# Optimization experiments

Hardware: AMD Instinct MI355X
Metric: run time of the kernel (lower is better)

Reference implementation:

```python
import jax, jax.numpy as jnp
import numpy as np
from jax import lax

B, S, C, H, T = 64, 256, 64, 512, 128  # batch, enc seq, coord_dims, hidden, target_len

def _lstm_step(Wih, Whh, b, h, c, xt):
    # PyTorch gate order: i, f, g, o
    g = xt @ Wih.T + h @ Whh.T + b
    i, f, gg, o = jnp.split(g, 4, axis=-1)
    i = jax.nn.sigmoid(i); f = jax.nn.sigmoid(f)
    gg = jnp.tanh(gg); o = jax.nn.sigmoid(o)
    c = f * c + i * gg
    h = o * jnp.tanh(c)
    return h, c

def _lstm_layer(x_seq, Wih, Whh, b):
    # x_seq: [B, S, D] -> outputs [B, S, H], final (h, c)
    Bsz = x_seq.shape[0]
    h0 = jnp.zeros((Bsz, Whh.shape[1]), x_seq.dtype)
    c0 = jnp.zeros_like(h0)
    def step(carry, xt):
        h, c = carry
        h, c = _lstm_step(Wih, Whh, b, h, c, xt)
        return (h, c), h
    (hT, cT), ys = lax.scan(step, (h0, c0), x_seq.swapaxes(0, 1))
    return ys.swapaxes(0, 1), hT, cT

def setup_inputs() -> dict:
    key = jax.random.key(0)
    ks = jax.random.split(key, 16)
    s = 1.0 / np.sqrt(H)
    def u(k, shape):
        return jax.random.uniform(k, shape, jnp.float32, -s, s)
    inp = {"x": jax.random.normal(ks[0], (B, S, C), jnp.float32), "target_len": T}
    inp["enc_Wih0"] = u(ks[1], (4 * H, C)); inp["enc_Whh0"] = u(ks[2], (4 * H, H)); inp["enc_b0"] = u(ks[3], (4 * H,))
    inp["enc_Wih1"] = u(ks[4], (4 * H, H)); inp["enc_Whh1"] = u(ks[5], (4 * H, H)); inp["enc_b1"] = u(ks[6], (4 * H,))
    inp["dec_Wih0"] = u(ks[7], (4 * H, C)); inp["dec_Whh0"] = u(ks[8], (4 * H, H)); inp["dec_b0"] = u(ks[9], (4 * H,))
    inp["dec_Wih1"] = u(ks[10], (4 * H, H)); inp["dec_Whh1"] = u(ks[11], (4 * H, H)); inp["dec_b1"] = u(ks[12], (4 * H,))
    inp["lin_W"] = u(ks[13], (C, H)); inp["lin_b"] = u(ks[14], (C,))
    return inp

def reference(x, enc_Wih0, enc_Whh0, enc_b0, enc_Wih1, enc_Whh1, enc_b1,
              dec_Wih0, dec_Whh0, dec_b0, dec_Wih1, dec_Whh1, dec_b1,
              lin_W, lin_b, target_len):
    # ---- encoder: 2-layer LSTM over full sequence ----
    y0, h0, c0 = _lstm_layer(x, enc_Wih0, enc_Whh0, enc_b0)
    _, h1, c1 = _lstm_layer(y0, enc_Wih1, enc_Whh1, enc_b1)
    dec_in0 = x[:, -1, :]  # [B, C]
    def step(carry, _):
        xin, h0_, c0_, h1_, c1_ = carry
        h0n, c0n = _lstm_step(dec_Wih0, dec_Whh0, dec_b0, h0_, c0_, xin)
        h1n, c1n = _lstm_step(dec_Wih1, dec_Whh1, dec_b1, h1_, c1_, h0n)
        out = h1n @ lin_W.T + lin_b  # [B, C]
        return (out, h0n, c0n, h1n, c1n), out
    _, outs = lax.scan(step, (dec_in0, h0, c0, h1, c1), None, length=target_len)
    return outs.swapaxes(0, 1)  # [B, target_len, C]
```

## Files before the change

### kernel.cpp

```cpp
#include <hip/hip_runtime.h>

typedef _Float16 f16;
typedef _Float16 f16x4 __attribute__((ext_vector_type(4)));
typedef _Float16 f16x8 __attribute__((ext_vector_type(8)));
typedef float    f32x4 __attribute__((ext_vector_type(4)));

#define MFMA16(a,b,c) __builtin_amdgcn_mfma_f32_16x16x32_f16((a),(b),(c),0,0,0)

constexpr unsigned NB = 64, NS = 256, NC = 64, NH = 512, NT = 128;
constexpr unsigned HSLOT = NB * NH;

constexpr unsigned OFF_WX   = 0;
constexpr unsigned OFF_WLIN = OFF_WX   + NB*NS*NC*2;
constexpr unsigned OFF_EH0  = OFF_WLIN + NC*NH*2;
constexpr unsigned OFF_EH1  = OFF_EH0  + 2*HSLOT*2;
constexpr unsigned OFF_DH0  = OFF_EH1  + 2*HSLOT*2;
constexpr unsigned OFF_DH1  = OFF_DH0  + 2*HSLOT*2;
constexpr unsigned OFF_BAR  = OFF_DH1  + 2*HSLOT*2;


__global__ void prep_convert(const float* __restrict__ x,
                             const float* __restrict__ linw,
                             char* __restrict__ ws)
{
    unsigned rel = blockIdx.x * 256u + threadIdx.x;
    if (rel < 65536u) {
        unsigned t = rel >> 8, c4 = (rel >> 4) & 15u, b0 = (rel & 15u) << 2;
        #pragma unroll
        for (unsigned j = 0; j < 4; ++j) {
            float4 v = ((const float4*)x)[(b0 + j) * 4096u + t * 16u + c4];
            f16x4 o; o[0]=(f16)v.x; o[1]=(f16)v.y; o[2]=(f16)v.z; o[3]=(f16)v.w;
            ((f16x4*)(ws + OFF_WX))[t * 1024u + c4 * 64u + b0 + j] = o;
        }
    } else if ((rel -= 65536u) < 8192u) {
        float4 v = ((const float4*)linw)[rel];
        f16x4 o; o[0]=(f16)v.x; o[1]=(f16)v.y; o[2]=(f16)v.z; o[3]=(f16)v.w;
        ((f16x4*)(ws + OFF_WLIN))[rel] = o;
    } else if ((rel -= 8192u) < 32768u) {
        f16x8 z = {};
        ((f16x8*)(ws + OFF_EH0))[rel] = z;
    } else if ((rel -= 32768u) < 512u) {
        int4 z; z.x = z.y = z.z = z.w = 0;
        ((int4*)(ws + OFF_BAR))[rel] = z;
    }
}


__device__ __forceinline__ float sigm(float v)   { return 1.f / (1.f + __expf(-v)); }
__device__ __forceinline__ float tanh_f(float v) { return 2.f / (1.f + __expf(-2.f * v)) - 1.f; }

__device__ __forceinline__ void h_store8(f16* p, f16x4 v)
{
    union { unsigned long long u; f16x4 h; } c; c.h = v;
    __hip_atomic_store((unsigned long long*)p, c.u, __ATOMIC_RELAXED, __HIP_MEMORY_SCOPE_AGENT);
}
__device__ __forceinline__ f16x4 h_load8(const f16* p)
{
    unsigned long long v = __hip_atomic_load((const unsigned long long*)p,
                                             __ATOMIC_RELAXED, __HIP_MEMORY_SCOPE_AGENT);
    union { unsigned long long u; f16x4 h; } c; c.u = v;
    return c.h;
}
__device__ __forceinline__ f16x8 h_load_blk(const f16* slot, int kr, int m)
{
    const f16* p = slot + ((kr >> 2) << 8) + (m << 2);
    f16x4 a = h_load8(p);
    f16x4 b = h_load8(p + 256);
    f16x8 r;
    r[0]=a[0]; r[1]=a[1]; r[2]=a[2]; r[3]=a[3];
    r[4]=b[0]; r[5]=b[1]; r[6]=b[2]; r[7]=b[3];
    return r;
}

__device__ __forceinline__ void grid_barrier(int* bar, int wg, int tid, int& bgen)
{
    __syncthreads();
    if (tid == 0) {
        const int g = wg >> 4;
        int* grp   = bar + g * 32;
        int* root  = bar + 16 * 32;
        int* flags = bar + 17 * 32;
        const int target = bgen + 1;

        int old = __hip_atomic_fetch_add(grp, 1, __ATOMIC_RELAXED, __HIP_MEMORY_SCOPE_AGENT);
        if ((old & 15) == 15) {
            int ro = __hip_atomic_fetch_add(root, 1, __ATOMIC_RELAXED, __HIP_MEMORY_SCOPE_AGENT);
            if ((ro & 15) == 15) {
                #pragma unroll
                for (int i = 0; i < 16; ++i)
                    __hip_atomic_store(flags + i * 32, target, __ATOMIC_RELAXED, __HIP_MEMORY_SCOPE_AGENT);
            }
        }
        int* myf = flags + g * 32;
        while (__hip_atomic_load(myf, __ATOMIC_RELAXED, __HIP_MEMORY_SCOPE_AGENT) < target)
            __builtin_amdgcn_s_sleep(1);
        bgen = target;
    }
    __syncthreads();
}

__device__ __forceinline__ void load_wlds_f32(f16 (*Wlds)[1032],
                                              const float* __restrict__ A, int KA,
                                              const float* __restrict__ Bs, int KB,
                                              int u0, int tid)
{
    int nch = (KA + KB) >> 2;
    int tot = nch << 6;
    for (int idx = tid; idx < tot; idx += 256) {
        int j = idx / nch, ch = idx - j * nch;
        int k = ch << 2;
        int grow = ((j >> 4) << 9) + u0 + (j & 15);
        float4 v;
        if (k < KA) v = *(const float4*)(A + grow * KA + k);
        else        v = *(const float4*)(Bs + grow * KB + (k - KA));
        f16x4 o; o[0]=(f16)v.x; o[1]=(f16)v.y; o[2]=(f16)v.z; o[3]=(f16)v.w;
        *(f16x4*)&Wlds[j][k] = o;
    }
}

__device__ __forceinline__ void load_wlds_fold(f16 (*Wlds)[1032],
                                               const float* __restrict__ dwih0,
                                               const float* __restrict__ linw,
                                               const float* __restrict__ dwhh0,
                                               int u0, int tid)
{
    #pragma unroll
    for (int rep = 0; rep < 4; ++rep) {
        int idx = ((rep << 8) + tid) << 5;
        int j = idx >> 9, k0 = idx & 511;
        int grow = ((j >> 4) << 9) + u0 + (j & 15);
        float acc[32];
        #pragma unroll
        for (int q = 0; q < 32; ++q) acc[q] = 0.f;
        for (int c = 0; c < 64; ++c) {
            float wc = dwih0[grow * 64 + c];
            const float* lr = linw + c * 512 + k0;
            #pragma unroll
            for (int q = 0; q < 32; ++q) acc[q] += wc * lr[q];
        }
        #pragma unroll
        for (int q = 0; q < 32; ++q) Wlds[j][k0 + q] = (f16)acc[q];
    }
    int tot = 8192;
    for (int idx = tid; idx < tot; idx += 256) {
        int j = idx >> 7, ch = idx & 127, k = ch << 2;
        int grow = ((j >> 4) << 9) + u0 + (j & 15);
        float4 v = *(const float4*)(dwhh0 + grow * 512 + k);
        f16x4 o; o[0]=(f16)v.x; o[1]=(f16)v.y; o[2]=(f16)v.z; o[3]=(f16)v.w;
        *(f16x4*)&Wlds[j][512 + k] = o;
    }
}

__device__ __forceinline__ void gemm_acc4(f16 (*Wlds)[1032],
                                          const f16* __restrict__ A0, int kOff,
                                          f32x4& ac0, f32x4& ac1, f32x4& ac2, f32x4& ac3,
                                          int b0, int tid)
{
    const int lane = tid & 63, wv = tid >> 6, q = lane >> 4, lo = lane & 15;
    const int s0 = wv << 2;
    f16x8 A[4];
    #pragma unroll
    for (int s = 0; s < 4; ++s) {
        int kr = ((s0 + s) << 5) + (q << 3);
        A[s] = h_load_blk(A0, kr, b0 + lo);
    }
    __builtin_amdgcn_sched_barrier(0);
    #pragma unroll
    for (int s = 0; s < 4; ++s) {
        int kk = kOff + ((s0 + s) << 5) + (q << 3);
        ac0 = MFMA16(A[s], *(const f16x8*)&Wlds[lo     ][kk], ac0);
        ac1 = MFMA16(A[s], *(const f16x8*)&Wlds[lo + 16][kk], ac1);
        ac2 = MFMA16(A[s], *(const f16x8*)&Wlds[lo + 32][kk], ac2);
        ac3 = MFMA16(A[s], *(const f16x8*)&Wlds[lo + 48][kk], ac3);
    }
}

__device__ __forceinline__ void finish_round(float (*Dp)[16][68],
                                             f32x4 ac0, f32x4 ac1, f32x4 ac2, f32x4 ac3,
                                             const float* ba, float& creg,
                                             f16* __restrict__ ho,
                                             int u0, int b0, int tid)
{
    const int lane = tid & 63, wv = tid >> 6, q = lane >> 4, lo = lane & 15;
    #pragma unroll
    for (int r = 0; r < 4; ++r) {
        int rr = (q << 2) + r;
        Dp[wv][rr][lo     ] = ac0[r];
        Dp[wv][rr][lo + 16] = ac1[r];
        Dp[wv][rr][lo + 32] = ac2[r];
        Dp[wv][rr][lo + 48] = ac3[r];
    }
    __syncthreads();
    const int b = tid >> 4, u = tid & 15;
    float v[4];
    #pragma unroll
    for (int g = 0; g < 4; ++g) {
        int col = (g << 4) + u;
        v[g] = Dp[0][b][col] + Dp[1][b][col] + Dp[2][b][col] + Dp[3][b][col] + ba[g];
    }
    float ii = sigm(v[0]), ff = sigm(v[1]), gg = tanh_f(v[2]), oo = sigm(v[3]);
    creg = ff * creg + ii * gg;
    float h = oo * tanh_f(creg);
    float h1 = __shfl_down(h, 1);
    float h2 = __shfl_down(h, 2);
    float h3 = __shfl_down(h, 3);
    if ((u & 3) == 0) {
        f16x4 hv; hv[0] = (f16)h; hv[1] = (f16)h1; hv[2] = (f16)h2; hv[3] = (f16)h3;
        h_store8(ho + (((u0 + u) >> 2) << 8) + ((b0 + b) << 2), hv);
    }
}

template<int MAXS, bool EXACT>
__device__ __forceinline__ void rnn_round(f16 (*Wlds)[1032], float (*Dp)[16][68],
                                          const f16* __restrict__ A0, int K0,
                                          const f16* __restrict__ A1,
                                          int K, int kStart,
                                          const float* ba, float& creg,
                                          f16* __restrict__ ho,
                                          int u0, int b0, int tid)
{
    const int lane = tid & 63, wv = tid >> 6, q = lane >> 4, lo = lane & 15;
    const int sBeg = kStart >> 5, n = (K >> 5) - sBeg;
    const int per = n >> 2, rem = n & 3;
    const int s0 = sBeg + wv * per + (wv < rem ? wv : rem);
    const int ns = EXACT ? MAXS : (per + (wv < rem ? 1 : 0));

    int sEff[MAXS];
    #pragma unroll
    for (int s = 0; s < MAXS; ++s)
        sEff[s] = s0 + (EXACT ? s : (s < ns ? s : ns - 1));

    f16x8 A[MAXS];
    #pragma unroll
    for (int s = 0; s < MAXS; ++s) {
        int kb = sEff[s] << 5;
        bool in0 = kb < K0;
        const f16* src = in0 ? A0 : A1;
        int kr = (in0 ? kb : kb - K0) + (q << 3);
        A[s] = h_load_blk(src, kr, b0 + lo);
    }
    if (!EXACT) {
        if (MAXS - 1 >= ns) { f16x8 z = {}; A[MAXS-1] = z; }
    }
    __builtin_amdgcn_sched_barrier(0);

    f32x4 ac0 = {0.f,0.f,0.f,0.f}, ac1 = ac0, ac2 = ac0, ac3 = ac0;
    #pragma unroll
    for (int s = 0; s < MAXS; ++s) {
        int kk = (sEff[s] << 5) + (q << 3);
        ac0 = MFMA16(A[s], *(const f16x8*)&Wlds[lo     ][kk], ac0);
        ac1 = MFMA16(A[s], *(const f16x8*)&Wlds[lo + 16][kk], ac1);
        ac2 = MFMA16(A[s], *(const f16x8*)&Wlds[lo + 32][kk], ac2);
        ac3 = MFMA16(A[s], *(const f16x8*)&Wlds[lo + 48][kk], ac3);
    }
    finish_round(Dp, ac0, ac1, ac2, ac3, ba, creg, ho, u0, b0, tid);
}

__device__ __forceinline__ void out_gemm(const f16* __restrict__ H1,
                                         const f16* __restrict__ LW,
                                         const float* __restrict__ linb,
                                         float* __restrict__ out,
                                         int w, int t, int tid)
{
    const int lane = tid & 63, wv = tid >> 6, q = lane >> 4, lo = lane & 15;
    int b0 = w << 4;
    f32x4 ac = {0.f,0.f,0.f,0.f};
    int c0 = wv << 4;

    f16x8 a[16];
    #pragma unroll
    for (int s = 0; s < 16; ++s)
        a[s] = h_load_blk(H1, (s << 5) + (q << 3), b0 + lo);
    __builtin_amdgcn_sched_barrier(0);

    #pragma unroll
    for (int s = 0; s < 16; ++s) {
        int kk = (s << 5) + (q << 3);
        f16x8 bf = *(const f16x8*)(LW + (c0 + lo) * 512 + kk);
        ac = MFMA16(a[s], bf, ac);
    }
    float lb = linb[c0 + lo];
    #pragma unroll
    for (int r = 0; r < 4; ++r) {
        int b = b0 + (q << 2) + r;
        out[(size_t)b * (NT * NC) + t * NC + c0 + lo] = ac[r] + lb;
    }
}


__global__ void __launch_bounds__(256)
lstm_main(char* __restrict__ ws,
          const float* __restrict__ x,
          const float* __restrict__ wih0, const float* __restrict__ whh0, const float* __restrict__ eb0,
          const float* __restrict__ wih1, const float* __restrict__ whh1, const float* __restrict__ eb1,
          const float* __restrict__ dwih0, const float* __restrict__ dwhh0, const float* __restrict__ db0,
          const float* __restrict__ dwih1, const float* __restrict__ dwhh1, const float* __restrict__ db1,
          const float* __restrict__ linw, const float* __restrict__ linb,
          float* __restrict__ out)
{
    __shared__ f16   Wlds[64][1032];
    __shared__ float Dp[4][16][68];

    const int wg = blockIdx.x, tid = threadIdx.x;
    const bool isL0 = wg < 128;
    const int wl = wg & 127;
    const int b0 = (wl & 3) << 4;
    const int u0 = (wl >> 2) << 4;
    const int u  = tid & 15;
    int* bar = (int*)(ws + OFF_BAR);
    int bgen = 0;

    const f16* WX   = (const f16*)(ws + OFF_WX);
    const f16* WLIN = (const f16*)(ws + OFF_WLIN);
    f16* EH0 = (f16*)(ws + OFF_EH0);
    f16* EH1 = (f16*)(ws + OFF_EH1);
    f16* DH0 = (f16*)(ws + OFF_DH0);
    f16* DH1 = (f16*)(ws + OFF_DH1);

    if (isL0) load_wlds_f32(Wlds, wih0,  64, whh0, 512, u0, tid);
    else      load_wlds_f32(Wlds, wih1, 512, whh1, 512, u0, tid);
    __syncthreads();

    float ba[4];
    {
        const float* bs = isL0 ? eb0 : eb1;
        #pragma unroll
        for (int g = 0; g < 4; ++g) ba[g] = bs[(g << 9) + u0 + u];
    }
    float creg = 0.f;

    for (int r = 0; r <= (int)NS; ++r) {
        if (isL0 && r < (int)NS) {
            rnn_round<5,false>(Wlds, Dp,
                      WX + r * 4096, 64,
                      EH0 + ((r + 1) & 1) * HSLOT,
                      576, 0, ba, creg,
                      EH0 + (r & 1) * HSLOT, u0, b0, tid);
        } else if (!isL0 && r >= 1) {
            int t = r - 1;
            rnn_round<8,true>(Wlds, Dp,
                      EH0 + (t & 1) * HSLOT, 512,
                      EH1 + ((t + 1) & 1) * HSLOT,
                      1024, 0, ba, creg,
                      EH1 + (t & 1) * HSLOT, u0, b0, tid);
        }
        grid_barrier(bar, wg, tid, bgen);
    }

    float baI[4];
    if (isL0) {
        load_wlds_fold(Wlds, dwih0, linw, dwhh0, u0, tid);
        const int bb = b0 + (tid >> 4);
        const float* xr = x + bb * (NS * NC) + (NS - 1) * NC;
        #pragma unroll
        for (int g = 0; g < 4; ++g) {
            int row = (g << 9) + u0 + u;
            const float* wr = dwih0 + row * 64;
            float bsum = 0.f, xsum = 0.f;
            for (int c = 0; c < 64; ++c) { bsum += linb[c] * wr[c]; xsum += xr[c] * wr[c]; }
            ba[g]  = db0[row] + bsum;
            baI[g] = db0[row] + xsum;
        }
    } else {
        load_wlds_f32(Wlds, dwih1, 512, dwhh1, 512, u0, tid);
        #pragma unroll
        for (int g = 0; g < 4; ++g) { ba[g] = db1[(g << 9) + u0 + u]; baI[g] = 0.f; }
    }
    __syncthreads();

    f32x4 c0 = {0.f,0.f,0.f,0.f}, c1 = c0, c2 = c0, c3 = c0;
    const f32x4 zero = {0.f,0.f,0.f,0.f};

    for (int d = 0; d < 2 * (int)NT; ++d) {
        int t = d >> 1;
        if ((d & 1) == 0) {
            if (isL0) {
                if (t == 0) {
                    f32x4 a0 = zero, a1 = zero, a2 = zero, a3 = zero;
                    gemm_acc4(Wlds, EH0 + HSLOT, 512, a0, a1, a2, a3, b0, tid);
                    finish_round(Dp, a0, a1, a2, a3, baI, creg, DH0, u0, b0, tid);
                } else {
                    f32x4 a0 = c0, a1 = c1, a2 = c2, a3 = c3;
                    gemm_acc4(Wlds, DH1 + ((t + 1) & 1) * HSLOT, 0, a0, a1, a2, a3, b0, tid);
                    finish_round(Dp, a0, a1, a2, a3, ba, creg,
                                 DH0 + (t & 1) * HSLOT, u0, b0, tid);
                }
            } else {
                const f16* h1p = (t == 0) ? EH1 + HSLOT : DH1 + ((t + 1) & 1) * HSLOT;
                c0 = zero; c1 = zero; c2 = zero; c3 = zero;
                gemm_acc4(Wlds, h1p, 512, c0, c1, c2, c3, b0, tid);
                if (wg < 132 && t >= 1)
                    out_gemm(DH1 + ((t - 1) & 1) * HSLOT, WLIN, linb, out, wg - 128, t - 1, tid);
            }
        } else {
            if (!isL0) {
                f32x4 a0 = c0, a1 = c1, a2 = c2, a3 = c3;
                gemm_acc4(Wlds, DH0 + (t & 1) * HSLOT, 0, a0, a1, a2, a3, b0, tid);
                finish_round(Dp, a0, a1, a2, a3, ba, creg,
                             DH1 + (t & 1) * HSLOT, u0, b0, tid);
            } else if (t < (int)NT - 1) {
                c0 = zero; c1 = zero; c2 = zero; c3 = zero;
                gemm_acc4(Wlds, DH0 + (t & 1) * HSLOT, 512, c0, c1, c2, c3, b0, tid);
            }
        }
        grid_barrier(bar, wg, tid, bgen);
    }

    if (!isL0 && wg < 132)
        out_gemm(DH1 + HSLOT, WLIN, linb, out, wg - 128, (int)NT - 1, tid);
}


extern "C" void kernel_launch(void* const* d_in, const int* in_sizes, int n_in,
                              void* d_out, int out_size, void* d_ws, size_t ws_size,
                              hipStream_t stream)
{
    const float* x     = (const float*)d_in[0];
    const float* wih0  = (const float*)d_in[2];
    const float* whh0  = (const float*)d_in[3];
    const float* eb0   = (const float*)d_in[4];
    const float* wih1  = (const float*)d_in[5];
    const float* whh1  = (const float*)d_in[6];
    const float* eb1   = (const float*)d_in[7];
    const float* dwih0 = (const float*)d_in[8];
    const float* dwhh0 = (const float*)d_in[9];
    const float* db0   = (const float*)d_in[10];
    const float* dwih1 = (const float*)d_in[11];
    const float* dwhh1 = (const float*)d_in[12];
    const float* db1   = (const float*)d_in[13];
    const float* linw  = (const float*)d_in[14];
    const float* linb  = (const float*)d_in[15];
    char* ws    = (char*)d_ws;
    float* outp = (float*)d_out;

    prep_convert<<<418, 256, 0, stream>>>(x, linw, ws);

    lstm_main<<<256, 256, 0, stream>>>(ws, x, wih0, whh0, eb0, wih1, whh1, eb1,
                                       dwih0, dwhh0, db0, dwih1, dwhh1, db1,
                                       linw, linb, outp);
}
```

Measured before the change: 2.092 ms.

## Replace global tree barrier with per-domain barriers over 64-workgroup subsets

The grid barrier used every recurrent step is restructured. Workgroups are split into 4 domains by wg&3, and each domain synchronises only its own 64 workgroups. Each domain has 4 monotonic sub-counters, each last arriver publishes a flag, and waiters poll the domain's 4 flags directly instead of going through a root counter and a broadcast. This removes one level of atomic serialisation and the cross-domain wait. It depends on domains being data-independent and on the larger barrier memory region being zeroed.

```diff
diff --git a/kernel.cpp b/kernel.cpp
--- a/kernel.cpp
+++ b/kernel.cpp
@@ -76,25 +76,25 @@
 {
     __syncthreads();
     if (tid == 0) {
-        const int g = wg >> 4;
-        int* grp   = bar + g * 32;
-        int* root  = bar + 16 * 32;
-        int* flags = bar + 17 * 32;
-        const int target = bgen + 1;
-
-        int old = __hip_atomic_fetch_add(grp, 1, __ATOMIC_RELAXED, __HIP_MEMORY_SCOPE_AGENT);
-        if ((old & 15) == 15) {
-            int ro = __hip_atomic_fetch_add(root, 1, __ATOMIC_RELAXED, __HIP_MEMORY_SCOPE_AGENT);
-            if ((ro & 15) == 15) {
-                #pragma unroll
-                for (int i = 0; i < 16; ++i)
-                    __hip_atomic_store(flags + i * 32, target, __ATOMIC_RELAXED, __HIP_MEMORY_SCOPE_AGENT);
-            }
-        }
-        int* myf = flags + g * 32;
-        while (__hip_atomic_load(myf, __ATOMIC_RELAXED, __HIP_MEMORY_SCOPE_AGENT) < target)
+        const int dom = wg & 3;
+        const int idx = ((wg >> 7) << 5) | ((wg >> 2) & 31);
+        const int sub = idx >> 4;
+        int* cnt  = bar + (dom * 4 + sub) * 32;
+        int* flg  = bar + 512 + (dom * 4) * 32;
+        const int gen = bgen + 1;
+
+        int old = __hip_atomic_fetch_add(cnt, 1, __ATOMIC_RELAXED, __HIP_MEMORY_SCOPE_AGENT);
+        if (old == (gen << 4) - 1)
+            __hip_atomic_store(flg + sub * 32, gen, __ATOMIC_RELAXED, __HIP_MEMORY_SCOPE_AGENT);
+        for (;;) {
+            int a = __hip_atomic_load(flg +  0, __ATOMIC_RELAXED, __HIP_MEMORY_SCOPE_AGENT);
+            int b = __hip_atomic_load(flg + 32, __ATOMIC_RELAXED, __HIP_MEMORY_SCOPE_AGENT);
+            int c = __hip_atomic_load(flg + 64, __ATOMIC_RELAXED, __HIP_MEMORY_SCOPE_AGENT);
+            int d = __hip_atomic_load(flg + 96, __ATOMIC_RELAXED, __HIP_MEMORY_SCOPE_AGENT);
+            if (a >= gen && b >= gen && c >= gen && d >= gen) break;
             __builtin_amdgcn_s_sleep(1);
-        bgen = target;
+        }
+        bgen = gen;
     }
     __syncthreads();
 }
```

New measurement: 1.923 ms. 1.09x faster.
